# Performance work log

Hardware: AMD Instinct MI355X
Metric: run time of the kernel (lower is better)

The kernel has to match this reference:

```python
import jax, jax.numpy as jnp
import numpy as np

B, H, S, D = 4, 16, 2048, 64

def setup_inputs() -> dict:
    key = jax.random.key(0)
    kq, kk, kv = jax.random.split(key, 3)
    return {
        "input_query": jax.random.normal(kq, (B, H, S, D), dtype=jnp.float32),
        "input_key": jax.random.normal(kk, (B, H, S, D), dtype=jnp.float32),
        "input_value": jax.random.normal(kv, (B, H, S, D), dtype=jnp.float32),
    }

def reference(input_query, input_key, input_value):
    # Unscaled, unmasked attention: softmax(Q K^T) V
    scores = jnp.einsum("bhsd,bhtd->bhst", input_query, input_key)  # [B,H,S,S]
    probs = jax.nn.softmax(scores, axis=-1)
    return jnp.einsum("bhst,bhtd->bhsd", probs, input_value)  # [B,H,S,D]
```

## Files before the change

kernel.cpp:

```cpp
#include <hip/hip_runtime.h>
#include <hip/hip_bf16.h>
#include <stdint.h>

#define SEQ 2048
#define DIM 64
#define NH  64
#define KT  32
#define NT  (SEQ / KT)
#define RAWK_BYTES 8192
#define FRAG_BYTES 12288
#define KF_BYTES   8192

typedef __attribute__((ext_vector_type(8)))  short    bf16x8;
typedef __attribute__((ext_vector_type(8)))  _Float16 f16x8;
typedef __attribute__((ext_vector_type(8)))  float    f32x8;
typedef __attribute__((ext_vector_type(16))) float    f32x16;
typedef unsigned int u32;

#if __has_builtin(__builtin_amdgcn_exp2f)
#define EXP2(x) __builtin_amdgcn_exp2f(x)
#else
#define EXP2(x) exp2f(x)
#endif

__device__ __forceinline__ int phi(int s) {
    int h = (s >> 2) & 1, b = s >> 3, i = s & 3;
    return 8 * h + 4 * b + i + (b >= 2 ? 8 : 0);
}

__global__ __launch_bounds__(384, 3) void attn_fused(
    const float* __restrict__ Q, const float* __restrict__ K,
    const float* __restrict__ V, float* __restrict__ O)
{
    __shared__ __align__(16) char rawK[3][RAWK_BYTES];
    __shared__ __align__(16) char frag[3][FRAG_BYTES];

    const int tid  = threadIdx.x;
    const int wave = tid >> 6, lane = tid & 63;
    const int h = lane >> 5, col = lane & 31;

    const int bid  = blockIdx.x;
    const int head = (bid & 7) * 8 + ((bid >> 3) & 7);
    const size_t base = (size_t)head * SEQ * DIM;

    if (wave < 4) {
        const int qw = (bid >> 6) * 256 + wave * 64;

        f16x8 qf[2][4];
        #pragma unroll
        for (int qt = 0; qt < 2; ++qt) {
            const float* qr = Q + base + (size_t)(qw + qt * 32 + col) * DIM;
            #pragma unroll
            for (int c = 0; c < 4; ++c)
                #pragma unroll
                for (int j = 0; j < 8; ++j)
                    qf[qt][c][j] = (_Float16)(qr[c * 16 + 8 * h + j] * 1.44269504088896f);
        }

        f32x16 z16;
        #pragma unroll
        for (int r = 0; r < 16; ++r) z16[r] = 0.f;
        f32x16 of[2][2];
        of[0][0] = z16; of[0][1] = z16; of[1][0] = z16; of[1][1] = z16;
        float l_own[2] = {0.f, 0.f};

        __builtin_amdgcn_s_barrier();

        int fi = 0;
        for (int kt = 0; kt < NT; ++kt) {
            asm volatile("s_waitcnt lgkmcnt(0)" ::: "memory");
            __builtin_amdgcn_s_barrier();
            __builtin_amdgcn_sched_barrier(0);
            const char* cur = frag[fi];

            f32x16 s[2]; s[0] = z16; s[1] = z16;
            __builtin_amdgcn_s_setprio(1);
            #pragma unroll
            for (int c = 0; c < 4; ++c) {
                f16x8 kh = *(const f16x8*)(cur + (c * 2 + 0) * 1024 + lane * 16);
                f16x8 kl = *(const f16x8*)(cur + (c * 2 + 1) * 1024 + lane * 16);
                s[0] = __builtin_amdgcn_mfma_f32_32x32x16_f16(kh, qf[0][c], s[0], 0, 0, 0);
                s[0] = __builtin_amdgcn_mfma_f32_32x32x16_f16(kl, qf[0][c], s[0], 0, 0, 0);
                s[1] = __builtin_amdgcn_mfma_f32_32x32x16_f16(kh, qf[1][c], s[1], 0, 0, 0);
                s[1] = __builtin_amdgcn_mfma_f32_32x32x16_f16(kl, qf[1][c], s[1], 0, 0, 0);
            }
            __builtin_amdgcn_s_setprio(0);

            bf16x8 pfrag[2][2];
            #pragma unroll
            for (int qt = 0; qt < 2; ++qt) {
                float p[16];
                #pragma unroll
                for (int r = 0; r < 16; ++r) p[r] = EXP2(s[qt][r]);
                float t0 = (p[0] + p[1]) + (p[2] + p[3]);
                float t1 = (p[4] + p[5]) + (p[6] + p[7]);
                float t2 = (p[8] + p[9]) + (p[10] + p[11]);
                float t3 = (p[12] + p[13]) + (p[14] + p[15]);
                l_own[qt] += (t0 + t1) + (t2 + t3);
                u32 pk[8];
                #pragma unroll
                for (int m = 0; m < 8; ++m) {
                    __hip_bfloat162 b2 = __float22bfloat162_rn(make_float2(p[2 * m], p[2 * m + 1]));
                    __builtin_memcpy(&pk[m], &b2, 4);
                }
                #pragma unroll
                for (int c = 0; c < 2; ++c) {
                    u32 a0 = pk[4 * c + 0], b0 = pk[4 * c + 2];
                    u32 a1 = pk[4 * c + 1], b1 = pk[4 * c + 3];
                    asm volatile("v_permlane32_swap_b32 %0, %1" : "+v"(a0), "+v"(b0));
                    asm volatile("v_permlane32_swap_b32 %0, %1" : "+v"(a1), "+v"(b1));
                    union { u32 w[4]; bf16x8 v; } fr;
                    fr.w[0] = a0; fr.w[1] = a1; fr.w[2] = b0; fr.w[3] = b1;
                    pfrag[qt][c] = fr.v;
                }
            }

            __builtin_amdgcn_s_setprio(1);
            #pragma unroll
            for (int f = 0; f < 2; ++f)
                #pragma unroll
                for (int c = 0; c < 2; ++c) {
                    bf16x8 vf = *(const bf16x8*)(cur + KF_BYTES + (f * 2 + c) * 1024 + lane * 16);
                    of[0][f] = __builtin_amdgcn_mfma_f32_32x32x16_bf16(pfrag[0][c], vf, of[0][f], 0, 0, 0);
                    of[1][f] = __builtin_amdgcn_mfma_f32_32x32x16_bf16(pfrag[1][c], vf, of[1][f], 0, 0, 0);
                }
            __builtin_amdgcn_s_setprio(0);

            fi = (fi == 2) ? 0 : fi + 1;
        }

        float* op = O + base;
        #pragma unroll
        for (int qt = 0; qt < 2; ++qt) {
            float lall = l_own[qt] + __shfl_xor(l_own[qt], 32);
            float inv = 1.0f / lall;
            #pragma unroll
            for (int r = 0; r < 16; ++r) {
                int qrow = (r & 3) + 8 * (r >> 2) + 4 * h;
                float iq = __shfl(inv, qrow);
                op[(size_t)(qw + qt * 32 + qrow) * DIM + col]      = of[qt][0][r] * iq;
                op[(size_t)(qw + qt * 32 + qrow) * DIM + 32 + col] = of[qt][1][r] * iq;
            }
        }
    } else {
        const int pw = wave - 4;
        const float* Kh = K + base;
        const float* Vh = V + base;

        const int fv = pw;
        int vrA[8], vrB[8];
        #pragma unroll
        for (int j = 0; j < 8; ++j) { vrA[j] = phi(8 * h + j); vrB[j] = phi(16 + 8 * h + j); }

        auto stageK = [&](int kt, char* dst) {
            const char* g = (const char*)(Kh + (size_t)kt * (KT * DIM));
            #pragma unroll
            for (int i = 0; i < 4; ++i) {
                const int P  = pw * 256 + i * 64 + lane;
                const int sk = (P & ~15) | ((P & 15) ^ ((P >> 4) & 7));
                char* d = dst + (size_t)(pw * 256 + i * 64) * 16;
                __builtin_amdgcn_global_load_lds(
                    (const __attribute__((address_space(1))) u32*)(g + (size_t)sk * 16),
                    (__attribute__((address_space(3))) u32*)d, 16, 0, 0);
            }
        };
        auto loadV = [&](int kt, f32x8& ra, f32x8& rb) {
            const float* vp = Vh + (size_t)kt * (KT * DIM) + fv * 32 + col;
            #pragma unroll
            for (int j = 0; j < 8; ++j) ra[j] = vp[vrA[j] * DIM];
            #pragma unroll
            for (int j = 0; j < 8; ++j) rb[j] = vp[vrB[j] * DIM];
        };
        auto convert = [&](const char* rk_, char* fr, f32x8 va, f32x8 vb) {
            const float4* rk4 = (const float4*)rk_;
            const int r = phi(col);
            #pragma unroll
            for (int cc = 0; cc < 2; ++cc) {
                const int c = 2 * pw + cc;
                const int kk = 4 * c + 2 * h;
                float4 a = rk4[r * 16 + ((kk    ) ^ (r & 7))];
                float4 b = rk4[r * 16 + ((kk + 1) ^ (r & 7))];
                float x[8] = {a.x, a.y, a.z, a.w, b.x, b.y, b.z, b.w};
                f16x8 hi, lo;
                #pragma unroll
                for (int j = 0; j < 8; ++j) {
                    _Float16 xh = (_Float16)x[j];
                    hi[j] = xh;
                    lo[j] = (_Float16)(x[j] - (float)xh);
                }
                *(f16x8*)(fr + (c * 2 + 0) * 1024 + lane * 16) = hi;
                *(f16x8*)(fr + (c * 2 + 1) * 1024 + lane * 16) = lo;
            }
            union { u32 w[4]; bf16x8 v; } ua, ub;
            #pragma unroll
            for (int j = 0; j < 4; ++j) {
                __hip_bfloat162 p2 = __float22bfloat162_rn(make_float2(va[2 * j], va[2 * j + 1]));
                __builtin_memcpy(&ua.w[j], &p2, 4);
                __hip_bfloat162 q2 = __float22bfloat162_rn(make_float2(vb[2 * j], vb[2 * j + 1]));
                __builtin_memcpy(&ub.w[j], &q2, 4);
            }
            *(bf16x8*)(fr + KF_BYTES + (fv * 2 + 0) * 1024 + lane * 16) = ua.v;
            *(bf16x8*)(fr + KF_BYTES + (fv * 2 + 1) * 1024 + lane * 16) = ub.v;
        };

        stageK(0, rawK[0]);
        stageK(1, rawK[1]);
        f32x8 a0, b0, a1, b1;
        loadV(0, a0, b0);
        loadV(1, a1, b1);
        asm volatile("s_waitcnt vmcnt(0)" ::: "memory");
        __builtin_amdgcn_s_barrier();
        convert(rawK[0], frag[0], a0, b0);
        convert(rawK[1], frag[1], a1, b1);
        stageK(2, rawK[2]);
        loadV(2, a0, b0);

        int ri = 2, si = 0;
        for (int kt = 0; kt < NT; ++kt) {
            asm volatile("s_waitcnt vmcnt(0) lgkmcnt(0)" ::: "memory");
            __builtin_amdgcn_s_barrier();
            __builtin_amdgcn_sched_barrier(0);

            const bool ld = (kt + 3 < NT);
            if (ld) stageK(kt + 3, rawK[si]);
            f32x8 na, nb;
            if (ld) loadV(kt + 3, na, nb);
            if (kt + 2 < NT)
                convert(rawK[ri], frag[ri], (kt & 1) ? a1 : a0, (kt & 1) ? b1 : b0);
            if (ld) { if (kt & 1) { a0 = na; b0 = nb; } else { a1 = na; b1 = nb; } }

            ri = (ri == 2) ? 0 : ri + 1;
            si = (si == 2) ? 0 : si + 1;
        }
    }
}

extern "C" void kernel_launch(void* const* d_in, const int* in_sizes, int n_in,
                              void* d_out, int out_size, void* d_ws, size_t ws_size,
                              hipStream_t stream) {
    const float* Q = (const float*)d_in[0];
    const float* K = (const float*)d_in[1];
    const float* V = (const float*)d_in[2];
    float* Out = (float*)d_out;
    (void)d_ws; (void)ws_size;

    attn_fused<<<dim3(NH * (SEQ / 256)), dim3(384), 0, stream>>>(Q, K, V, Out);
}
```

Before: 278.4 us.

## Use four producer waves with double-buffered LDS to fit more blocks per CU

Block size grows from 384 to 512 threads, giving four producer waves instead of two. Each producer now stages half as many K chunks, converts one K column group and fills one V fragment half. The K/V staging ring shrinks from triple to double buffering, which cuts LDS per block so four blocks can be resident per CU. The goal is more concurrent consumer waves and more parallel conversion work. In exchange, prefetch depth drops by one tile, so load latency is less hidden and the extra waves put more pressure on registers.

```diff
diff --git a/kernel.cpp b/kernel.cpp
--- a/kernel.cpp
+++ b/kernel.cpp
@@ -28,12 +28,12 @@
     return 8 * h + 4 * b + i + (b >= 2 ? 8 : 0);
 }
 
-__global__ __launch_bounds__(384, 3) void attn_fused(
+__global__ __launch_bounds__(512, 4) void attn_fused(
     const float* __restrict__ Q, const float* __restrict__ K,
     const float* __restrict__ V, float* __restrict__ O)
 {
-    __shared__ __align__(16) char rawK[3][RAWK_BYTES];
-    __shared__ __align__(16) char frag[3][FRAG_BYTES];
+    __shared__ __align__(16) char rawK[2][RAWK_BYTES];
+    __shared__ __align__(16) char frag[2][FRAG_BYTES];
 
     const int tid  = threadIdx.x;
     const int wave = tid >> 6, lane = tid & 63;
@@ -66,12 +66,11 @@
 
         __builtin_amdgcn_s_barrier();
 
-        int fi = 0;
         for (int kt = 0; kt < NT; ++kt) {
             asm volatile("s_waitcnt lgkmcnt(0)" ::: "memory");
             __builtin_amdgcn_s_barrier();
             __builtin_amdgcn_sched_barrier(0);
-            const char* cur = frag[fi];
+            const char* cur = frag[kt & 1];
 
             f32x16 s[2]; s[0] = z16; s[1] = z16;
             __builtin_amdgcn_s_setprio(1);
@@ -125,8 +124,6 @@
                     of[1][f] = __builtin_amdgcn_mfma_f32_32x32x16_bf16(pfrag[1][c], vf, of[1][f], 0, 0, 0);
                 }
             __builtin_amdgcn_s_setprio(0);
-
-            fi = (fi == 2) ? 0 : fi + 1;
         }
 
         float* op = O + base;
@@ -147,90 +144,78 @@
         const float* Kh = K + base;
         const float* Vh = V + base;
 
-        const int fv = pw;
-        int vrA[8], vrB[8];
-        #pragma unroll
-        for (int j = 0; j < 8; ++j) { vrA[j] = phi(8 * h + j); vrB[j] = phi(16 + 8 * h + j); }
+        const int fv = pw >> 1, cv = pw & 1;
+        int vrow[8];
+        #pragma unroll
+        for (int j = 0; j < 8; ++j) vrow[j] = phi(16 * cv + 8 * h + j);
 
         auto stageK = [&](int kt, char* dst) {
             const char* g = (const char*)(Kh + (size_t)kt * (KT * DIM));
             #pragma unroll
-            for (int i = 0; i < 4; ++i) {
-                const int P  = pw * 256 + i * 64 + lane;
+            for (int i = 0; i < 2; ++i) {
+                const int P  = pw * 128 + i * 64 + lane;
                 const int sk = (P & ~15) | ((P & 15) ^ ((P >> 4) & 7));
-                char* d = dst + (size_t)(pw * 256 + i * 64) * 16;
+                char* d = dst + (size_t)(pw * 128 + i * 64) * 16;
                 __builtin_amdgcn_global_load_lds(
                     (const __attribute__((address_space(1))) u32*)(g + (size_t)sk * 16),
                     (__attribute__((address_space(3))) u32*)d, 16, 0, 0);
             }
         };
-        auto loadV = [&](int kt, f32x8& ra, f32x8& rb) {
+        auto loadV = [&](int kt) -> f32x8 {
             const float* vp = Vh + (size_t)kt * (KT * DIM) + fv * 32 + col;
-            #pragma unroll
-            for (int j = 0; j < 8; ++j) ra[j] = vp[vrA[j] * DIM];
-            #pragma unroll
-            for (int j = 0; j < 8; ++j) rb[j] = vp[vrB[j] * DIM];
+            f32x8 r;
+            #pragma unroll
+            for (int j = 0; j < 8; ++j) r[j] = vp[vrow[j] * DIM];
+            return r;
         };
-        auto convert = [&](const char* rk_, char* fr, f32x8 va, f32x8 vb) {
+        auto convert = [&](const char* rk_, char* fr, f32x8 vv) {
+            const int r = phi(col);
+            const int kk = 4 * pw + 2 * h;
             const float4* rk4 = (const float4*)rk_;
-            const int r = phi(col);
-            #pragma unroll
-            for (int cc = 0; cc < 2; ++cc) {
-                const int c = 2 * pw + cc;
-                const int kk = 4 * c + 2 * h;
-                float4 a = rk4[r * 16 + ((kk    ) ^ (r & 7))];
-                float4 b = rk4[r * 16 + ((kk + 1) ^ (r & 7))];
-                float x[8] = {a.x, a.y, a.z, a.w, b.x, b.y, b.z, b.w};
-                f16x8 hi, lo;
-                #pragma unroll
-                for (int j = 0; j < 8; ++j) {
-                    _Float16 xh = (_Float16)x[j];
-                    hi[j] = xh;
-                    lo[j] = (_Float16)(x[j] - (float)xh);
-                }
-                *(f16x8*)(fr + (c * 2 + 0) * 1024 + lane * 16) = hi;
-                *(f16x8*)(fr + (c * 2 + 1) * 1024 + lane * 16) = lo;
-            }
-            union { u32 w[4]; bf16x8 v; } ua, ub;
+            float4 a = rk4[r * 16 + ((kk    ) ^ (r & 7))];
+            float4 b = rk4[r * 16 + ((kk + 1) ^ (r & 7))];
+            float x[8] = {a.x, a.y, a.z, a.w, b.x, b.y, b.z, b.w};
+            f16x8 hi, lo;
+            #pragma unroll
+            for (int j = 0; j < 8; ++j) {
+                _Float16 xh = (_Float16)x[j];
+                hi[j] = xh;
+                lo[j] = (_Float16)(x[j] - (float)xh);
+            }
+            *(f16x8*)(fr + (pw * 2 + 0) * 1024 + lane * 16) = hi;
+            *(f16x8*)(fr + (pw * 2 + 1) * 1024 + lane * 16) = lo;
+            union { u32 w[4]; bf16x8 v; } uv;
             #pragma unroll
             for (int j = 0; j < 4; ++j) {
-                __hip_bfloat162 p2 = __float22bfloat162_rn(make_float2(va[2 * j], va[2 * j + 1]));
-                __builtin_memcpy(&ua.w[j], &p2, 4);
-                __hip_bfloat162 q2 = __float22bfloat162_rn(make_float2(vb[2 * j], vb[2 * j + 1]));
-                __builtin_memcpy(&ub.w[j], &q2, 4);
-            }
-            *(bf16x8*)(fr + KF_BYTES + (fv * 2 + 0) * 1024 + lane * 16) = ua.v;
-            *(bf16x8*)(fr + KF_BYTES + (fv * 2 + 1) * 1024 + lane * 16) = ub.v;
+                __hip_bfloat162 b2 = __float22bfloat162_rn(make_float2(vv[2 * j], vv[2 * j + 1]));
+                __builtin_memcpy(&uv.w[j], &b2, 4);
+            }
+            *(bf16x8*)(fr + KF_BYTES + (fv * 2 + cv) * 1024 + lane * 16) = uv.v;
         };
 
         stageK(0, rawK[0]);
-        stageK(1, rawK[1]);
-        f32x8 a0, b0, a1, b1;
-        loadV(0, a0, b0);
-        loadV(1, a1, b1);
+        f32x8 vv0 = loadV(0);
         asm volatile("s_waitcnt vmcnt(0)" ::: "memory");
         __builtin_amdgcn_s_barrier();
-        convert(rawK[0], frag[0], a0, b0);
-        convert(rawK[1], frag[1], a1, b1);
-        stageK(2, rawK[2]);
-        loadV(2, a0, b0);
-
-        int ri = 2, si = 0;
+        convert(rawK[0], frag[0], vv0);
+        stageK(1, rawK[1]);
+        f32x8 vvE, vvO;
+        vvO = loadV(1);
+
         for (int kt = 0; kt < NT; ++kt) {
             asm volatile("s_waitcnt vmcnt(0) lgkmcnt(0)" ::: "memory");
             __builtin_amdgcn_s_barrier();
             __builtin_amdgcn_sched_barrier(0);
 
-            const bool ld = (kt + 3 < NT);
-            if (ld) stageK(kt + 3, rawK[si]);
-            f32x8 na, nb;
-            if (ld) loadV(kt + 3, na, nb);
-            if (kt + 2 < NT)
-                convert(rawK[ri], frag[ri], (kt & 1) ? a1 : a0, (kt & 1) ? b1 : b0);
-            if (ld) { if (kt & 1) { a0 = na; b0 = nb; } else { a1 = na; b1 = nb; } }
-
-            ri = (ri == 2) ? 0 : ri + 1;
-            si = (si == 2) ? 0 : si + 1;
+            const bool ld = (kt + 2 < NT);
+            if (ld) stageK(kt + 2, rawK[kt & 1]);
+            f32x8 vn;
+            if (ld) vn = loadV(kt + 2);
+            if (kt + 1 < NT)
+                convert(rawK[(kt + 1) & 1], frag[(kt + 1) & 1],
+                        ((kt + 1) & 1) ? vvO : vvE);
+            if (ld) { if (kt & 1) vvO = vn; else vvE = vn; }
+
         }
     }
 }
@@ -244,5 +229,5 @@
     float* Out = (float*)d_out;
     (void)d_ws; (void)ws_size;
 
-    attn_fused<<<dim3(NH * (SEQ / 256)), dim3(384), 0, stream>>>(Q, K, V, Out);
+    attn_fused<<<dim3(NH * (SEQ / 256)), dim3(512), 0, stream>>>(Q, K, V, Out);
 }
```

Result: slower. 298.4 us (+7.2%).
